# Kernel tuning notes

Hardware: AMD Instinct MI355X
Metric: run time of the kernel (lower is better)

## Reference

```python
import jax, jax.numpy as jnp
import numpy as np

NMS_THRESH = 0.3  # default nms_thresh in DetNet.predict


def setup_inputs() -> dict:
    key = jax.random.key(0)
    k1, k2, k3, k4 = jax.random.split(key, 4)
    W, N = 8, 1024
    det = jax.random.uniform(k1, (W, N, 5), dtype=jnp.float32)          # (conf, cx, cy, w, h) in [0,1)
    offsets = jax.random.uniform(k2, (W, 5), dtype=jnp.float32) * 0.5   # window offset vector (0, left, top, 0, 0)-like
    scales = jax.random.uniform(k3, (W, 5), dtype=jnp.float32) * 0.5 + 0.25  # window scale vector
    b = jax.random.uniform(k4, (W, 4), dtype=jnp.float32)
    # (valid_left, valid_right, valid_top, valid_bottom) with left<right, top<bottom
    bounds = jnp.stack([0.3 * b[:, 0], 0.7 + 0.3 * b[:, 1],
                        0.3 * b[:, 2], 0.7 + 0.3 * b[:, 3]], axis=-1)
    return {"det": det, "offsets": offsets, "scales": scales, "bounds": bounds}


def _pairwise_iou(boxes):
    # boxes: [M,4] in (x1,y1,x2,y2)
    x1, y1, x2, y2 = boxes[:, 0], boxes[:, 1], boxes[:, 2], boxes[:, 3]
    area = jnp.clip(x2 - x1, 0.0) * jnp.clip(y2 - y1, 0.0)              # [M]
    iw = jnp.clip(jnp.minimum(x2[:, None], x2[None, :]) - jnp.maximum(x1[:, None], x1[None, :]), 0.0)
    ih = jnp.clip(jnp.minimum(y2[:, None], y2[None, :]) - jnp.maximum(y1[:, None], y1[None, :]), 0.0)
    inter = iw * ih                                                     # [M,M]
    union = area[:, None] + area[None, :] - inter
    return inter / jnp.maximum(union, 1e-9)


def reference(det, offsets, scales, bounds):
    W, N, _ = det.shape
    M = W * N
    cx, cy = det[..., 1], det[..., 2]                                    # [W,N]
    left, right = bounds[:, 0:1], bounds[:, 1:2]
    top, bottom = bounds[:, 2:3], bounds[:, 3:4]
    valid = (cx < right) & (cx > left) & (cy < bottom) & (cy > top)      # [W,N] border mask
    # torch.addcmul(offset, d, scale) = offset + d * scale
    d = (offsets[:, None, :] + det * scales[:, None, :]).reshape(M, 5)
    valid = valid.reshape(M)
    scores = jnp.where(valid, d[:, 0], -1.0)                             # invalid boxes never kept
    order = jnp.argsort(-scores)                                         # descending confidence
    d_s = d[order]                                                       # [M,5]
    s_s = scores[order]
    # point_form: (cx,cy,w,h) -> (x1,y1,x2,y2)
    cxy, wh = d_s[:, 1:3], d_s[:, 3:5]
    boxes = jnp.concatenate([cxy - wh * 0.5, cxy + wh * 0.5], axis=-1)
    iou = jax.lax.stop_gradient(_pairwise_iou(boxes))                    # [M,M], suppression is non-diff
    s_c = jax.lax.stop_gradient(s_s)
    idx = jnp.arange(M)

    def body(i, keep):
        # suppressed if any kept higher-score box overlaps > thresh
        sup = jnp.any(keep & (idx < i) & (iou[:, i] > NMS_THRESH))
        return keep.at[i].set(jnp.logical_and(~sup, s_c[i] > 0.0))

    keep = jax.lax.fori_loop(0, M, body, jnp.ones((M,), dtype=bool))
    return d_s * keep[:, None].astype(d_s.dtype)                         # [M,5], suppressed rows zeroed
```

## Files before the change

kernel.cpp:

```cpp
#include <hip/hip_runtime.h>
#include <cstdint>


#define M_TOT 8192
#define NMS_T 0.3f

#define WS_BOX   65536
#define WS_D     196608
#define WS_VCNT  360448
#define WS_ZROW  393216
#define WS_MASK  524288

typedef unsigned long long u64t;

__device__ __forceinline__ uint32_t desc_key(float sv) {
    uint32_t u = __float_as_uint(sv);
    uint32_t m = (u & 0x80000000u) ? ~u : (u | 0x80000000u);
    return ~m;
}

__device__ __forceinline__ u64t rdl64(u64t v, int sl) {
    unsigned lo = (unsigned)__builtin_amdgcn_readlane((int)(unsigned)v, sl);
    unsigned hi = (unsigned)__builtin_amdgcn_readlane((int)(unsigned)(v >> 32), sl);
    return ((u64t)hi << 32) | lo;
}

__device__ __forceinline__ int scatter_one(
    int i, int rank, u64t key,
    const float* __restrict__ det, const float* __restrict__ offsets,
    const float* __restrict__ scales,
    float4* __restrict__ boxes_srt, float* __restrict__ d_srt)
{
    uint32_t dkey = (uint32_t)(key >> 16);
    if (dkey >= 0x7FFFFFFFu) return 0;
    int g = i >> 10;
    float d0 = __fadd_rn(offsets[g*5+0], __fmul_rn(det[i*5+0], scales[g*5+0]));
    float d1 = __fadd_rn(offsets[g*5+1], __fmul_rn(det[i*5+1], scales[g*5+1]));
    float d2 = __fadd_rn(offsets[g*5+2], __fmul_rn(det[i*5+2], scales[g*5+2]));
    float d3 = __fadd_rn(offsets[g*5+3], __fmul_rn(det[i*5+3], scales[g*5+3]));
    float d4 = __fadd_rn(offsets[g*5+4], __fmul_rn(det[i*5+4], scales[g*5+4]));
    d_srt[rank*5+0] = d0; d_srt[rank*5+1] = d1; d_srt[rank*5+2] = d2;
    d_srt[rank*5+3] = d3; d_srt[rank*5+4] = d4;
    float hw = __fmul_rn(d3, 0.5f), hh = __fmul_rn(d4, 0.5f);
    boxes_srt[rank] = make_float4(__fsub_rn(d1, hw), __fsub_rn(d2, hh),
                                  __fadd_rn(d1, hw), __fadd_rn(d2, hh));
    return 1;
}

__global__ __launch_bounds__(256) void k2_rank(
    const float* __restrict__ det, const float* __restrict__ offsets,
    const float* __restrict__ scales, const float* __restrict__ bounds,
    float4* __restrict__ boxes_srt, float* __restrict__ d_srt,
    unsigned int* __restrict__ vcnt, u64t* __restrict__ zrow,
    float* __restrict__ out)
{
    __shared__ u64t skey[M_TOT];
    __shared__ float soff[40], sscl[40], sbnd[32];
    __shared__ int sTop;
    int t = threadIdx.x;
    int lane = t & 63;
    if (t == 0) sTop = 0;
    if (t < 40) { soff[t] = offsets[t]; sscl[t] = scales[t]; }
    if (t < 32) { sbnd[t] = bounds[t]; }
    if (blockIdx.x == 0 && t < 128) zrow[t] = 0ull;
    __syncthreads();

    #pragma unroll 4
    for (int s = 0; s < 32; ++s) {
        int u = s * 256 + t;
        int g = u >> 10;
        float raw_s = det[u * 5 + 0];
        float cx    = det[u * 5 + 1];
        float cy    = det[u * 5 + 2];
        float score = __fadd_rn(soff[g * 5 + 0], __fmul_rn(raw_s, sscl[g * 5 + 0]));
        bool valid = (cx < sbnd[g*4+1]) && (cx > sbnd[g*4+0]) &&
                     (cy < sbnd[g*4+3]) && (cy > sbnd[g*4+2]);
        float sv = valid ? score : -1.0f;
        uint32_t dk = desc_key(sv);
        bool push = dk < 0x7FFFFFFFu;
        u64t key = ((u64t)dk << 16) | (unsigned)u;
        u64t bal = __ballot(push);
        if (bal) {
            int lw = 0;
            if (lane == 0) lw = atomicAdd(&sTop, __popcll(bal));
            int wbase = __builtin_amdgcn_readfirstlane(lw);
            if (push) {
                int off = __popcll(bal & ((1ull << lane) - 1ull));
                skey[wbase + off] = key;
            }
        }
    }
    __syncthreads();
    int V = sTop;
    int Vpad = (V + 15) & ~15;
    if (t < Vpad - V) skey[V + t] = ~0ull;
    {
        int zb = blockIdx.x * 160;
        for (int z = zb + t; z < zb + 160; z += 256) out[z] = 0.0f;
    }
    __syncthreads();
    if (t == 0) *vcnt = (unsigned)V;

    int grp = t >> 3;
    int jq  = t & 7;
    int i = blockIdx.x * 32 + grp;
    int g = i >> 10;
    float raw_s = det[i * 5 + 0];
    float cx    = det[i * 5 + 1];
    float cy    = det[i * 5 + 2];
    float score = __fadd_rn(soff[g * 5 + 0], __fmul_rn(raw_s, sscl[g * 5 + 0]));
    bool valid = (cx < sbnd[g*4+1]) && (cx > sbnd[g*4+0]) &&
                 (cy < sbnd[g*4+3]) && (cy > sbnd[g*4+2]);
    float sv = valid ? score : -1.0f;
    uint32_t dk = desc_key(sv);
    u64t ki = ((u64t)dk << 16) | (unsigned)i;
    const ulonglong2* skey2 = (const ulonglong2*)skey;
    int c = 0;
    int nit = Vpad >> 4;
    #pragma unroll 4
    for (int it = 0; it < nit; ++it) {
        ulonglong2 kj = skey2[it * 8 + jq];
        c += (kj.x < ki) + (kj.y < ki);
    }
    c += __shfl_xor(c, 1);
    c += __shfl_xor(c, 2);
    c += __shfl_xor(c, 4);
    if (jq == 0)
        scatter_one(i, c, ki, det, offsets, scales, boxes_srt, d_srt);
}

__global__ __launch_bounds__(256) void k_mask(
    const float4* __restrict__ boxes_srt,
    const unsigned int* __restrict__ vcnt,
    u64t* __restrict__ mask)
{
    __shared__ float4 sb[16 * 65];
    __shared__ float  sa[16 * 65];
    int V = (int)*vcnt;
    int bx = blockIdx.x, by = blockIdx.y;
    if (bx * 32 >= V) return;
    if (by * 1024 >= V) return;
    if (by * 16 + 15 < (bx * 32) >> 6) return;
    int nc = (V + 63) >> 6;
    int tid = threadIdx.x;
    int cbase = by * 1024;
    for (int u = tid; u < 1024; u += 256) {
        float4 b = boxes_srt[cbase + u];
        int c = u >> 6, jj = u & 63;
        sb[c * 65 + jj] = b;
        sa[c * 65 + jj] = __fmul_rn(fmaxf(__fsub_rn(b.z, b.x), 0.0f),
                                    fmaxf(__fsub_rn(b.w, b.y), 0.0f));
    }
    __syncthreads();
    int r = bx * 32 + (tid >> 3);
    if (r >= V) return;
    float4 bi = boxes_srt[r];
    float ai = __fmul_rn(fmaxf(__fsub_rn(bi.z, bi.x), 0.0f),
                         fmaxf(__fsub_rn(bi.w, bi.y), 0.0f));
    int rw = r >> 6;
    #pragma unroll
    for (int k = 0; k < 2; ++k) {
        int wl = (tid & 7) + k * 8;
        int w = by * 16 + wl;
        if (w < rw || w >= nc) continue;
        u64t bits = 0;
        #pragma unroll 4
        for (int jj = 0; jj < 64; ++jj) {
            float4 bj = sb[wl * 65 + jj];
            float aj = sa[wl * 65 + jj];
            float iw = fmaxf(__fsub_rn(fminf(bi.z, bj.z), fmaxf(bi.x, bj.x)), 0.0f);
            float ih = fmaxf(__fsub_rn(fminf(bi.w, bj.w), fmaxf(bi.y, bj.y)), 0.0f);
            float inter = __fmul_rn(iw, ih);
            float uni   = __fsub_rn(__fadd_rn(ai, aj), inter);
            float iou   = __fdiv_rn(inter, fmaxf(uni, 1e-9f));
            int j = w * 64 + jj;
            if (j > r && iou > NMS_T) bits |= 1ull << jj;
        }
        mask[(size_t)r * 128 + w] = bits;
    }
}

struct WSlot { ulonglong2 dl, dh, n1l, n1h, n2l, n2h; };

__device__ __forceinline__ void fill_words(
    const u64t* __restrict__ mask, int lane, int T, WSlot& w)
{
    int rl = min(T * 128 + lane,      M_TOT - 1);
    int rh = min(T * 128 + 64 + lane, M_TOT - 1);
    const ulonglong2* mrl = (const ulonglong2*)(mask + (size_t)rl * 128);
    const ulonglong2* mrh = (const ulonglong2*)(mask + (size_t)rh * 128);
    int p0 = min(T,     63);
    int p1 = min(T + 1, 63);
    int p2 = min(T + 2, 63);
    w.dl  = mrl[p0]; w.dh  = mrh[p0];
    w.n1l = mrl[p1]; w.n1h = mrh[p1];
    w.n2l = mrl[p2]; w.n2h = mrh[p2];
}

__device__ __forceinline__ void step(
    const u64t* __restrict__ mask, const u64t* __restrict__ zrow,
    u64t* ck, int lane, int V, int nc, int T,
    u64t& r0, u64t& r1,
    u64t& cA_lo, u64t& cA_hi, u64t& cB_lo, u64t& cB_hi,
    ulonglong2 (&p)[16], WSlot& w)
{
    int base = T * 128;
    u64t a0 = 0, a1 = 0;
    #pragma unroll
    for (int q = 0; q < 16; ++q) { a0 |= p[q].x; a1 |= p[q].y; }
    r0 |= a0; r1 |= a1;
    u64t live_lo = ~(rdl64(r0, T) | cA_lo);
    u64t live_hi = ~(rdl64(r1, T) | cA_hi);
    int rem = V - base;
    if (rem < 128) {
        live_lo &= (rem >= 64) ? ~0ull : ((1ull << rem) - 1ull);
        int rh = rem - 64;
        live_hi &= (rh >= 64) ? ~0ull : ((rh <= 0) ? 0ull : ((1ull << rh) - 1ull));
    }
    u64t km_lo = 0, km_hi = 0, c1l = 0, c1h = 0, c2l = 0, c2h = 0;
    while (live_lo | live_hi) {
        if (live_lo) {
            int bs = __builtin_amdgcn_readfirstlane(__builtin_ctzll(live_lo));
            u64t rml = rdl64(w.dl.x, bs), rmh = rdl64(w.dl.y, bs);
            c1l |= rdl64(w.n1l.x, bs); c1h |= rdl64(w.n1l.y, bs);
            c2l |= rdl64(w.n2l.x, bs); c2h |= rdl64(w.n2l.y, bs);
            km_lo |= 1ull << bs;
            live_lo &= ~rml & ~(1ull << bs);
            live_hi &= ~rmh;
        } else {
            int bs = __builtin_amdgcn_readfirstlane(__builtin_ctzll(live_hi));
            u64t rmh = rdl64(w.dh.y, bs);
            c1l |= rdl64(w.n1h.x, bs); c1h |= rdl64(w.n1h.y, bs);
            c2l |= rdl64(w.n2h.x, bs); c2h |= rdl64(w.n2h.y, bs);
            km_hi |= 1ull << bs;
            live_hi &= ~rmh & ~(1ull << bs);
        }
    }
    if (lane == 0) { ck[2 * T] = km_lo; ck[2 * T + 1] = km_hi; }
    cA_lo = cB_lo | c1l; cA_hi = cB_hi | c1h;
    cB_lo = c2l;         cB_hi = c2h;
    u64t kl = km_lo, kh = km_hi;
    #pragma unroll
    for (int q = 0; q < 16; ++q) {
        const ulonglong2* ptr;
        if (kl) {
            int b = __builtin_ctzll(kl); kl &= kl - 1;
            ptr = (const ulonglong2*)(mask + (size_t)(base + b) * 128) + lane;
        } else if (kh) {
            int b = __builtin_ctzll(kh); kh &= kh - 1;
            ptr = (const ulonglong2*)(mask + (size_t)(base + 64 + b) * 128) + lane;
        } else {
            ptr = (const ulonglong2*)zrow + lane;
        }
        p[q] = *ptr;
    }
    if (kl | kh) {
        while (kl) {
            int b = __builtin_ctzll(kl); kl &= kl - 1;
            ulonglong2 s = *((const ulonglong2*)(mask + (size_t)(base + b) * 128) + lane);
            r0 |= s.x; r1 |= s.y;
        }
        while (kh) {
            int b = __builtin_ctzll(kh); kh &= kh - 1;
            ulonglong2 s = *((const ulonglong2*)(mask + (size_t)(base + 64 + b) * 128) + lane);
            r0 |= s.x; r1 |= s.y;
        }
    }
    fill_words(mask, lane, T + 3, w);
}

__global__ __launch_bounds__(64) void k3_serial(
    const u64t* __restrict__ mask, const u64t* __restrict__ zrow,
    const float* __restrict__ d_srt, const unsigned int* __restrict__ vcnt,
    float* __restrict__ out)
{
    __shared__ u64t ck[128];
    int lane = threadIdx.x;
    int V = (int)*vcnt;
    int nc = (V + 127) >> 7;
    ck[lane] = 0ull; ck[64 + lane] = 0ull;
    u64t r0 = 0, r1 = 0;
    u64t cA_lo = 0, cA_hi = 0, cB_lo = 0, cB_hi = 0;
    ulonglong2 pA[16], pB[16], pC[16];
    #pragma unroll
    for (int q = 0; q < 16; ++q) {
        pA[q] = ulonglong2{0, 0}; pB[q] = ulonglong2{0, 0}; pC[q] = ulonglong2{0, 0};
    }
    WSlot WA, WB, WC;
    fill_words(mask, lane, 0, WA);
    fill_words(mask, lane, 1, WB);
    fill_words(mask, lane, 2, WC);
    for (int t = 0; t < nc; t += 3) {
        step(mask, zrow, ck, lane, V, nc, t,     r0, r1, cA_lo, cA_hi, cB_lo, cB_hi, pA, WA);
        if (t + 1 < nc)
            step(mask, zrow, ck, lane, V, nc, t + 1, r0, r1, cA_lo, cA_hi, cB_lo, cB_hi, pB, WB);
        if (t + 2 < nc)
            step(mask, zrow, ck, lane, V, nc, t + 2, r0, r1, cA_lo, cA_hi, cB_lo, cB_hi, pC, WC);
    }
    __syncthreads();
    #pragma unroll
    for (int h = 0; h < 2; ++h) {
        u64t m = ck[h * 64 + lane];
        while (m) {
            int b = __builtin_ctzll(m); m &= m - 1;
            int rr = (h * 64 + lane) * 64 + b;
            out[rr * 5 + 0] = d_srt[rr * 5 + 0];
            out[rr * 5 + 1] = d_srt[rr * 5 + 1];
            out[rr * 5 + 2] = d_srt[rr * 5 + 2];
            out[rr * 5 + 3] = d_srt[rr * 5 + 3];
            out[rr * 5 + 4] = d_srt[rr * 5 + 4];
        }
    }
}

extern "C" void kernel_launch(void* const* d_in, const int* in_sizes, int n_in,
                              void* d_out, int out_size, void* d_ws, size_t ws_size,
                              hipStream_t stream) {
    const float* det     = (const float*)d_in[0];
    const float* offsets = (const float*)d_in[1];
    const float* scales  = (const float*)d_in[2];
    const float* bounds  = (const float*)d_in[3];
    float* out = (float*)d_out;
    char* ws = (char*)d_ws;
    float4*       boxes = (float4*)(ws + WS_BOX);
    float*        d_srt = (float*)(ws + WS_D);
    unsigned int* vcnt  = (unsigned int*)(ws + WS_VCNT);
    u64t*         zrow  = (u64t*)(ws + WS_ZROW);
    u64t*         mask  = (u64t*)(ws + WS_MASK);

    k2_rank<<<256, 256, 0, stream>>>(det, offsets, scales, bounds, boxes, d_srt, vcnt, zrow, out);
    k_mask<<<dim3(256, 8), 256, 0, stream>>>(boxes, vcnt, mask);
    k3_serial<<<1, 64, 0, stream>>>(mask, zrow, d_srt, vcnt, out);
}
```

Before: 160.1 us.

## Split serial NMS into resolver wave and seven helper waves OR-ing kept rows

```diff
diff --git a/kernel.cpp b/kernel.cpp
--- a/kernel.cpp
+++ b/kernel.cpp
@@ -197,26 +197,23 @@
     w.n2l = mrl[p2]; w.n2h = mrh[p2];
 }
 
-__device__ __forceinline__ void step(
-    const u64t* __restrict__ mask, const u64t* __restrict__ zrow,
-    u64t* ck, int lane, int V, int nc, int T,
-    u64t& r0, u64t& r1,
-    u64t& cA_lo, u64t& cA_hi, u64t& cB_lo, u64t& cB_hi,
-    ulonglong2 (&p)[16], WSlot& w)
-{
-    int base = T * 128;
-    u64t a0 = 0, a1 = 0;
-    #pragma unroll
-    for (int q = 0; q < 16; ++q) { a0 |= p[q].x; a1 |= p[q].y; }
-    r0 |= a0; r1 |= a1;
-    u64t live_lo = ~(rdl64(r0, T) | cA_lo);
-    u64t live_hi = ~(rdl64(r1, T) | cA_hi);
-    int rem = V - base;
-    if (rem < 128) {
-        live_lo &= (rem >= 64) ? ~0ull : ((1ull << rem) - 1ull);
-        int rh = rem - 64;
-        live_hi &= (rh >= 64) ? ~0ull : ((rh <= 0) ? 0ull : ((1ull << rh) - 1ull));
-    }
+__device__ __forceinline__ void res_step(
+    const u64t* __restrict__ mask,
+    u64t* sdead, u64t* ck, volatile int* res_prog, volatile int* h_prog,
+    int lane, int nc, int T,
+    u64t& cA_lo, u64t& cA_hi, u64t& cB_lo, u64t& cB_hi, WSlot& w)
+{
+    if (T >= 3) {
+        int need = T - 2;
+        while (true) {
+            int hp = (lane < 7) ? h_prog[lane] : 0x7FFFFFFF;
+            if (__ballot(hp < need) == 0ull) break;
+        }
+    }
+    u64t dlo = ((volatile u64t*)sdead)[2 * T];
+    u64t dhi = ((volatile u64t*)sdead)[2 * T + 1];
+    u64t live_lo = ~(dlo | cA_lo);
+    u64t live_hi = ~(dhi | cA_hi);
     u64t km_lo = 0, km_hi = 0, c1l = 0, c1h = 0, c2l = 0, c2h = 0;
     while (live_lo | live_hi) {
         if (live_lo) {
@@ -237,73 +234,95 @@
         }
     }
     if (lane == 0) { ck[2 * T] = km_lo; ck[2 * T + 1] = km_hi; }
+    __threadfence_block();
+    if (lane == 0) *res_prog = T + 1;
     cA_lo = cB_lo | c1l; cA_hi = cB_hi | c1h;
     cB_lo = c2l;         cB_hi = c2h;
-    u64t kl = km_lo, kh = km_hi;
-    #pragma unroll
-    for (int q = 0; q < 16; ++q) {
-        const ulonglong2* ptr;
-        if (kl) {
-            int b = __builtin_ctzll(kl); kl &= kl - 1;
-            ptr = (const ulonglong2*)(mask + (size_t)(base + b) * 128) + lane;
-        } else if (kh) {
-            int b = __builtin_ctzll(kh); kh &= kh - 1;
-            ptr = (const ulonglong2*)(mask + (size_t)(base + 64 + b) * 128) + lane;
-        } else {
-            ptr = (const ulonglong2*)zrow + lane;
-        }
-        p[q] = *ptr;
-    }
-    if (kl | kh) {
-        while (kl) {
-            int b = __builtin_ctzll(kl); kl &= kl - 1;
-            ulonglong2 s = *((const ulonglong2*)(mask + (size_t)(base + b) * 128) + lane);
-            r0 |= s.x; r1 |= s.y;
-        }
-        while (kh) {
-            int b = __builtin_ctzll(kh); kh &= kh - 1;
-            ulonglong2 s = *((const ulonglong2*)(mask + (size_t)(base + 64 + b) * 128) + lane);
-            r0 |= s.x; r1 |= s.y;
-        }
-    }
     fill_words(mask, lane, T + 3, w);
 }
 
-__global__ __launch_bounds__(64) void k3_serial(
+__global__ __launch_bounds__(512) void k3_serial(
     const u64t* __restrict__ mask, const u64t* __restrict__ zrow,
     const float* __restrict__ d_srt, const unsigned int* __restrict__ vcnt,
     float* __restrict__ out)
 {
+    __shared__ u64t sdead[128];
     __shared__ u64t ck[128];
-    int lane = threadIdx.x;
+    __shared__ int  res_prog;
+    __shared__ int  h_prog[7];
+    int tid = threadIdx.x, wv = tid >> 6, lane = tid & 63;
     int V = (int)*vcnt;
     int nc = (V + 127) >> 7;
-    ck[lane] = 0ull; ck[64 + lane] = 0ull;
-    u64t r0 = 0, r1 = 0;
-    u64t cA_lo = 0, cA_hi = 0, cB_lo = 0, cB_hi = 0;
-    ulonglong2 pA[16], pB[16], pC[16];
-    #pragma unroll
-    for (int q = 0; q < 16; ++q) {
-        pA[q] = ulonglong2{0, 0}; pB[q] = ulonglong2{0, 0}; pC[q] = ulonglong2{0, 0};
-    }
-    WSlot WA, WB, WC;
-    fill_words(mask, lane, 0, WA);
-    fill_words(mask, lane, 1, WB);
-    fill_words(mask, lane, 2, WC);
-    for (int t = 0; t < nc; t += 3) {
-        step(mask, zrow, ck, lane, V, nc, t,     r0, r1, cA_lo, cA_hi, cB_lo, cB_hi, pA, WA);
-        if (t + 1 < nc)
-            step(mask, zrow, ck, lane, V, nc, t + 1, r0, r1, cA_lo, cA_hi, cB_lo, cB_hi, pB, WB);
-        if (t + 2 < nc)
-            step(mask, zrow, ck, lane, V, nc, t + 2, r0, r1, cA_lo, cA_hi, cB_lo, cB_hi, pC, WC);
-    }
-    __syncthreads();
-    #pragma unroll
-    for (int h = 0; h < 2; ++h) {
-        u64t m = ck[h * 64 + lane];
+    if (tid < 128) {
+        int bw = tid * 64;
+        u64t w0 = 0;
+        if (bw >= V)           w0 = ~0ull;
+        else if (bw + 64 > V)  w0 = (~0ull) << (V - bw);
+        sdead[tid] = w0;
+        ck[tid] = 0ull;
+    }
+    if (tid == 0) res_prog = 0;
+    if (tid < 7)  h_prog[tid] = tid;
+    __syncthreads();
+
+    if (wv == 0) {
+        u64t cA_lo = 0, cA_hi = 0, cB_lo = 0, cB_hi = 0;
+        WSlot WA, WB, WC;
+        fill_words(mask, lane, 0, WA);
+        fill_words(mask, lane, 1, WB);
+        fill_words(mask, lane, 2, WC);
+        for (int t = 0; t < nc; t += 3) {
+            res_step(mask, sdead, ck, &res_prog, h_prog, lane, nc, t,
+                     cA_lo, cA_hi, cB_lo, cB_hi, WA);
+            if (t + 1 < nc)
+                res_step(mask, sdead, ck, &res_prog, h_prog, lane, nc, t + 1,
+                         cA_lo, cA_hi, cB_lo, cB_hi, WB);
+            if (t + 2 < nc)
+                res_step(mask, sdead, ck, &res_prog, h_prog, lane, nc, t + 2,
+                         cA_lo, cA_hi, cB_lo, cB_hi, WC);
+        }
+    } else {
+        int hh = wv - 1;
+        for (int c = hh; c < nc; c += 7) {
+            while (*(volatile int*)&res_prog <= c) __builtin_amdgcn_s_sleep(1);
+            u64t kl = ((volatile u64t*)ck)[2 * c];
+            u64t kh = ((volatile u64t*)ck)[2 * c + 1];
+            if (kl | kh) {
+                int base = c * 128;
+                u64t ax = 0, ay = 0;
+                while (kl | kh) {
+                    ulonglong2 b[4];
+                    #pragma unroll
+                    for (int q = 0; q < 4; ++q) {
+                        const ulonglong2* ptr;
+                        if (kl) {
+                            int b_ = __builtin_ctzll(kl); kl &= kl - 1;
+                            ptr = (const ulonglong2*)(mask + (size_t)(base + b_) * 128) + lane;
+                        } else if (kh) {
+                            int b_ = __builtin_ctzll(kh); kh &= kh - 1;
+                            ptr = (const ulonglong2*)(mask + (size_t)(base + 64 + b_) * 128) + lane;
+                        } else {
+                            ptr = (const ulonglong2*)zrow + lane;
+                        }
+                        b[q] = *ptr;
+                    }
+                    ax |= b[0].x | b[1].x | b[2].x | b[3].x;
+                    ay |= b[0].y | b[1].y | b[2].y | b[3].y;
+                }
+                atomicOr(&sdead[2 * lane],     ax);
+                atomicOr(&sdead[2 * lane + 1], ay);
+            }
+            __threadfence_block();
+            if (lane == 0) ((volatile int*)h_prog)[hh] = c + 7;
+        }
+        if (lane == 0) ((volatile int*)h_prog)[hh] = 0x7FFFFFFF;
+    }
+    __syncthreads();
+    if (tid < 128) {
+        u64t m = ck[tid];
         while (m) {
             int b = __builtin_ctzll(m); m &= m - 1;
-            int rr = (h * 64 + lane) * 64 + b;
+            int rr = tid * 64 + b;
             out[rr * 5 + 0] = d_srt[rr * 5 + 0];
             out[rr * 5 + 1] = d_srt[rr * 5 + 1];
             out[rr * 5 + 2] = d_srt[rr * 5 + 2];
@@ -330,5 +349,5 @@
 
     k2_rank<<<256, 256, 0, stream>>>(det, offsets, scales, bounds, boxes, d_srt, vcnt, zrow, out);
     k_mask<<<dim3(256, 8), 256, 0, stream>>>(boxes, vcnt, mask);
-    k3_serial<<<1, 64, 0, stream>>>(mask, zrow, d_srt, vcnt, out);
-}
+    k3_serial<<<1, 512, 0, stream>>>(mask, zrow, d_srt, vcnt, out);
+}
```

Result: no change. 162.0 us (+1.2%).
